# Performance work log

Measured on AMD Instinct MI355X. Metric: run time of the kernel, lower is better.

## Reference

```python
import jax, jax.numpy as jnp
import numpy as np

TOP_K = 2
EPS = 1e-10


def setup_inputs() -> dict:
    key = jax.random.key(0)
    k1, k2, k3, k4 = jax.random.split(key, 4)
    B, S, H, E = 4, 2048, 1024, 8
    tokens = jax.random.normal(k1, (B, S, H), dtype=jnp.float32)
    router_w = jax.random.normal(k2, (E, H), dtype=jnp.float32) * (1.0 / np.sqrt(H))
    router_b = jax.random.normal(k3, (E,), dtype=jnp.float32) * 0.01
    expert_weights = jax.random.normal(k4, (E, H, H), dtype=jnp.float32) * (1.0 / np.sqrt(H))
    return {"tokens": tokens, "router_w": router_w, "router_b": router_b,
            "expert_weights": expert_weights}


def reference(tokens, router_w, router_b, expert_weights):
    B, S, H = tokens.shape
    E = expert_weights.shape[0]
    # Router (torch Linear: x @ W^T + b)
    logits = jnp.einsum('bsh,eh->bse', tokens, router_w) + router_b  # [B,S,E]
    probs = jax.nn.softmax(logits, axis=-1)
    top_p, top_i = jax.lax.top_k(probs, TOP_K)            # [B,S,K]
    w = top_p / (jnp.sum(top_p, axis=-1, keepdims=True) + EPS)  # normalized weights

    x = tokens.reshape(-1, H)                              # [N,H]
    idx = top_i.reshape(-1, TOP_K)                         # [N,K]
    wf = w.reshape(-1, TOP_K)                              # [N,K]

    # Expert GEMM: compute all experts then gather selected (dense, vectorized
    # equivalent of the sort/pad/grouped-GEMM dispatch; padded rows with
    # original_indices==-1 never contribute to the output).
    y_all = jnp.einsum('nh,ehd->ned', x, expert_weights)   # [N,E,H]
    y_k = jnp.take_along_axis(y_all, idx[:, :, None], axis=1)  # [N,K,H]

    out = jnp.einsum('nk,nkh->nh', wf, y_k)                # weighted combine
    acc = jnp.clip(jnp.sum(wf, axis=-1), EPS, None)        # weight accumulator
    out = (out / acc[:, None]).reshape(B, S, H)

    # epsilon scale tying output to normalized router probs (gradient path)
    scale = 1.0 + jnp.sum(w, axis=-1, keepdims=True) * EPS  # [B,S,1]
    return out * scale
```

## Files before the change

kernel.cpp:

```cpp
#include <hip/hip_runtime.h>
#include <stdint.h>

#define N_TOK 8192
#define H_DIM 1024
#define N_EXP 8
#define MAX_TILES 136

typedef __bf16 bf16x8 __attribute__((ext_vector_type(8)));
typedef float floatx4 __attribute__((ext_vector_type(4)));

typedef __attribute__((address_space(1))) void GV;
typedef __attribute__((address_space(3))) void LV;

static __device__ __forceinline__ unsigned short f2b(float f) {
    union { float f; unsigned int i; } v; v.f = f;
    unsigned int u = v.i;
    return (unsigned short)((u + 0x7FFFu + ((u >> 16) & 1u)) >> 16);
}
static __device__ __forceinline__ float b2f(unsigned short u) {
    union { unsigned int i; float f; } v; v.i = ((unsigned int)u) << 16; return v.f;
}

__global__ __launch_bounds__(256) void k_front(
    const float* __restrict__ tokens,
    const float* __restrict__ router_w,
    const float* __restrict__ router_b,
    const float* __restrict__ W,
    int* __restrict__ sel, float* __restrict__ w_arr,
    unsigned short* __restrict__ tokb,
    unsigned short* __restrict__ Bp)
{
    const int t = threadIdx.x;

    if (blockIdx.x >= 2048) {
        const int idx = blockIdx.x - 2048;
        const int kg = idx & 127;
        const int e  = idx >> 7;
        const int d  = t * 4;
        const float* src = W + ((size_t)e * H_DIM + kg * 8) * H_DIM + d;
        float col[8][4];
#pragma unroll
        for (int j = 0; j < 8; ++j) {
            float4 v = *(const float4*)(src + (size_t)j * H_DIM);
            col[j][0] = v.x; col[j][1] = v.y; col[j][2] = v.z; col[j][3] = v.w;
        }
        unsigned short* dst = Bp + ((size_t)(e * 128 + kg) * H_DIM + d) * 8;
#pragma unroll
        for (int k = 0; k < 4; ++k) {
            unsigned short v[8];
#pragma unroll
            for (int j = 0; j < 8; ++j) v[j] = f2b(col[j][k]);
            *(uint4*)(dst + (size_t)k * 8) = *(uint4*)v;
        }
        return;
    }

    const int wave = t >> 6;
    const int lane = t & 63;
    const int n = blockIdx.x * 4 + wave;

    const float* xp = tokens + (size_t)n * H_DIM + lane * 16;
    float x[16];
#pragma unroll
    for (int i = 0; i < 4; ++i) {
        float4 v = *(const float4*)(xp + i * 4);
        x[i * 4 + 0] = v.x; x[i * 4 + 1] = v.y; x[i * 4 + 2] = v.z; x[i * 4 + 3] = v.w;
    }

    {
        unsigned short xb[16];
#pragma unroll
        for (int j = 0; j < 16; ++j) xb[j] = f2b(x[j]);
        unsigned short* dp = tokb + (size_t)n * H_DIM + lane * 16;
        *(uint4*)(dp)     = *(uint4*)(xb);
        *(uint4*)(dp + 8) = *(uint4*)(xb + 8);
    }

    float acc[N_EXP];
#pragma unroll
    for (int e = 0; e < N_EXP; ++e) {
        const float* wp = router_w + e * H_DIM + lane * 16;
        float s = 0.f;
#pragma unroll
        for (int i = 0; i < 4; ++i) {
            float4 v = *(const float4*)(wp + i * 4);
            s += x[i * 4 + 0] * v.x + x[i * 4 + 1] * v.y
               + x[i * 4 + 2] * v.z + x[i * 4 + 3] * v.w;
        }
        acc[e] = s;
    }

#pragma unroll
    for (int e = 0; e < N_EXP; ++e) {
        float a = acc[e];
#pragma unroll
        for (int off = 32; off > 0; off >>= 1) a += __shfl_xor(a, off);
        acc[e] = a;
    }

    if (lane == 0) {
        float lg[N_EXP];
#pragma unroll
        for (int e = 0; e < N_EXP; ++e) lg[e] = acc[e] + router_b[e];
        int e0 = 0;
#pragma unroll
        for (int e = 1; e < N_EXP; ++e) if (lg[e] > lg[e0]) e0 = e;
        int e1 = -1;
#pragma unroll
        for (int e = 0; e < N_EXP; ++e) {
            if (e == e0) continue;
            if (e1 < 0 || lg[e] > lg[e1]) e1 = e;
        }
        float w0 = 1.f / (1.f + __expf(lg[e1] - lg[e0]));
        float w1 = 1.f - w0;
        sel[n] = e0 | (e1 << 4);
        w_arr[n * 2] = w0;
        w_arr[n * 2 + 1] = w1;
    }
}

__global__ __launch_bounds__(256) void k_scan(
    const int* __restrict__ sel, int* __restrict__ cnt, int* __restrict__ bucket)
{
    __shared__ int ssel[N_TOK + N_TOK / 32];
    __shared__ int sc[256];
    const int e = blockIdx.x;
    const int t = threadIdx.x;
#pragma unroll
    for (int i = 0; i < 32; ++i) {
        int n = i * 256 + t;
        ssel[n + (n >> 5)] = sel[n];
    }
    __syncthreads();
    const int base = t * 32;
    int c = 0;
#pragma unroll
    for (int i = 0; i < 32; ++i) {
        int n = base + i;
        int s = ssel[n + (n >> 5)];
        c += ((s & 15) == e) + (((s >> 4) & 15) == e);
    }
    sc[t] = c;
    __syncthreads();
    for (int off = 1; off < 256; off <<= 1) {
        int v = (t >= off) ? sc[t - off] : 0;
        __syncthreads();
        sc[t] += v;
        __syncthreads();
    }
    int pos = sc[t] - c;
    if (t == 255) cnt[e] = sc[255];
#pragma unroll
    for (int i = 0; i < 32; ++i) {
        int n = base + i;
        int s = ssel[n + (n >> 5)];
        if ((s & 15) == e)        bucket[e * N_TOK + pos++] = 2 * n;
        if (((s >> 4) & 15) == e) bucket[e * N_TOK + pos++] = 2 * n + 1;
    }
}

__global__ __launch_bounds__(256, 2) void k_gemm(
    const unsigned short* __restrict__ tokb,
    const unsigned short* __restrict__ Bp,
    const int* __restrict__ cnt, const int* __restrict__ bucket,
    unsigned short* __restrict__ Y)
{
    const int nt = blockIdx.x & 7;
    const int tile = blockIdx.x >> 3;
    int base = 0, e = 0, mt = -1;
#pragma unroll
    for (int ee = 0; ee < 8; ++ee) {
        int te = (cnt[ee] + 127) >> 7;
        if (tile >= base && tile < base + te) { e = ee; mt = tile - base; }
        base += te;
    }
    if (mt < 0) return;
    const int cnt_local = cnt[e] - mt * 128;

    __shared__ __align__(16) unsigned short Asm[2][128 * 64];
    __shared__ __align__(16) unsigned short Bsm[2][8 * 128 * 8];
    __shared__ int rows[128];

    const int t = threadIdx.x;
    if (t < 128)
        rows[t] = (t < cnt_local) ? bucket[e * N_TOK + mt * 128 + t] : -1;
    __syncthreads();

    const int wv = t >> 6, lane = t & 63;
    const int d0 = nt * 128;

    const int p_sw = (lane & 7) ^ ((lane >> 3) & 7);
    const unsigned short* aptr[4];
#pragma unroll
    for (int i = 0; i < 4; ++i) {
        int r = i * 32 + wv * 8 + (lane >> 3);
        int rid = rows[r];
        int tok = (rid >= 0) ? (rid >> 1) : 0;
        aptr[i] = tokb + (size_t)tok * H_DIM + p_sw * 8;
    }
    const unsigned short* bbase = Bp
        + ((size_t)(e * 128 + (t >> 7)) * H_DIM + d0 + (t & 127)) * 8;

    const int w_row = wv >> 1, w_col = wv & 1;
    const int m_lane = lane & 15, quad = lane >> 4;
    const int r7 = m_lane & 7;

    floatx4 acc[4][4];
#pragma unroll
    for (int i = 0; i < 4; ++i)
#pragma unroll
        for (int j = 0; j < 4; ++j) acc[i][j] = (floatx4){0.f, 0.f, 0.f, 0.f};

#pragma unroll
    for (int i = 0; i < 4; ++i) {
        __builtin_amdgcn_global_load_lds(
            (GV*)(aptr[i]), (LV*)(&Asm[0][i * 2048 + wv * 512]), 16, 0, 0);
        __builtin_amdgcn_global_load_lds(
            (GV*)(bbase + (size_t)i * 16384), (LV*)(&Bsm[0][i * 2048 + wv * 512]), 16, 0, 0);
    }
    asm volatile("s_waitcnt vmcnt(0)" ::: "memory");
    __builtin_amdgcn_s_barrier();
    asm volatile("" ::: "memory");

    for (int kt = 0; kt < H_DIM / 64; ++kt) {
        const int cb = kt & 1;
        if (kt < H_DIM / 64 - 1) {
#pragma unroll
            for (int i = 0; i < 4; ++i) {
                __builtin_amdgcn_global_load_lds(
                    (GV*)(aptr[i] + (kt + 1) * 64),
                    (LV*)(&Asm[cb ^ 1][i * 2048 + wv * 512]), 16, 0, 0);
                __builtin_amdgcn_global_load_lds(
                    (GV*)(bbase + (size_t)i * 16384 + (size_t)(kt + 1) * 65536),
                    (LV*)(&Bsm[cb ^ 1][i * 2048 + wv * 512]), 16, 0, 0);
            }
        }

#pragma unroll
        for (int s = 0; s < 2; ++s) {
            bf16x8 a[4], b[4];
#pragma unroll
            for (int i = 0; i < 4; ++i) {
                int row = w_row * 64 + i * 16 + m_lane;
                a[i] = *(const bf16x8*)&Asm[cb][row * 64 + ((s * 4 + quad) ^ r7) * 8];
            }
#pragma unroll
            for (int j = 0; j < 4; ++j)
                b[j] = *(const bf16x8*)&Bsm[cb][((s * 4 + quad) * 128 + w_col * 64 + j * 16 + m_lane) * 8];
#pragma unroll
            for (int i = 0; i < 4; ++i)
#pragma unroll
                for (int j = 0; j < 4; ++j)
                    acc[i][j] = __builtin_amdgcn_mfma_f32_16x16x32_bf16(a[i], b[j], acc[i][j], 0, 0, 0);
        }

        asm volatile("s_waitcnt vmcnt(0)" ::: "memory");
        __builtin_amdgcn_s_barrier();
        asm volatile("" ::: "memory");
    }

#pragma unroll
    for (int i = 0; i < 4; ++i) {
        const int lr_base = w_row * 64 + i * 16 + quad * 4;
#pragma unroll
        for (int reg = 0; reg < 4; ++reg) {
            const int lr = lr_base + reg;
            const int rid = rows[lr];
            if (rid >= 0) {
                unsigned short v[4];
#pragma unroll
                for (int j = 0; j < 4; ++j) v[j] = f2b(acc[i][j][reg]);
                *(uint2*)(Y + (size_t)rid * H_DIM + d0 + w_col * 64 + m_lane * 4) = *(uint2*)v;
            }
        }
    }
}

__global__ __launch_bounds__(256) void k_combine(
    const unsigned short* __restrict__ Y, const float* __restrict__ w_arr,
    float* __restrict__ out)
{
    __shared__ __align__(16) unsigned short Ys[4 * H_DIM];
    const int t = threadIdx.x;
    const int b = blockIdx.x;
    const int wv = t >> 6, lane = t & 63;
    const unsigned short* src = Y + (size_t)b * 4 * H_DIM;
#pragma unroll
    for (int r = 0; r < 2; ++r) {
        __builtin_amdgcn_global_load_lds(
            (GV*)(src + (size_t)r * 2048 + wv * 512 + lane * 8),
            (LV*)(&Ys[r * 2048 + wv * 512]), 16, 0, 0);
    }
    __syncthreads();

    const int tok = t >> 7;
    const int n = 2 * b + tok;
    const int d0 = (t & 127) * 8;
    const int seg = d0 >> 7;
    const int dseg = d0 & 127;
    const int wc = dseg >> 6;
    const int j  = (dseg >> 4) & 3;
    const int m0 = dseg & 15;
    const int sbase = tok * 2 * H_DIM + seg * 128 + wc * 64 + j;
    const float w0 = w_arr[2 * n], w1 = w_arr[2 * n + 1];

    float o[8];
#pragma unroll
    for (int k = 0; k < 8; ++k) {
        int s = sbase + (m0 + k) * 4;
        o[k] = w0 * b2f(Ys[s]) + w1 * b2f(Ys[s + H_DIM]);
    }
    float4* op = (float4*)(out + (size_t)n * H_DIM + d0);
    op[0] = make_float4(o[0], o[1], o[2], o[3]);
    op[1] = make_float4(o[4], o[5], o[6], o[7]);
}

extern "C" void kernel_launch(void* const* d_in, const int* in_sizes, int n_in,
                              void* d_out, int out_size, void* d_ws, size_t ws_size,
                              hipStream_t stream)
{
    const float* tokens   = (const float*)d_in[0];
    const float* router_w = (const float*)d_in[1];
    const float* router_b = (const float*)d_in[2];
    const float* W        = (const float*)d_in[3];
    float* out = (float*)d_out;

    char* ws = (char*)d_ws;
    int*   cnt    = (int*)(ws);
    int*   sel    = (int*)(ws + 1024);
    float* w_arr  = (float*)(ws + 34816);
    int*   bucket = (int*)(ws + 100352);
    unsigned short* tokb = (unsigned short*)(ws + 362496);
    unsigned short* Bp   = (unsigned short*)(ws + 17139712);
    unsigned short* Y    = (unsigned short*)(ws + 33916928);

    k_front  <<<2048 + 1024, 256, 0, stream>>>(tokens, router_w, router_b, W,
                                               sel, w_arr, tokb, Bp);
    k_scan   <<<N_EXP, 256, 0, stream>>>(sel, cnt, bucket);
    k_gemm   <<<MAX_TILES * 8, 256, 0, stream>>>(tokb, Bp, cnt, bucket, Y);
    k_combine<<<N_TOK * (H_DIM / 8) / 256, 256, 0, stream>>>(Y, w_arr, out);
}
```

Baseline: 218.1 us.

## Shrink grouped GEMM tiles to 64x128 with persistent grid-stride scheduling

The expert GEMM moves from 128x128 tiles with 256 threads to 64x128 tiles with 128 threads, launched on a fixed persistent grid of 1056 blocks that loop over work items. The smaller M tile is meant to cut padding waste in each expert's last tile and to allow three blocks per CU. In exchange it drops LDS double buffering, so each k-step loads and then computes behind two barriers. It also halves A-tile reuse per B load and reads bucket indices straight from global memory instead of shared memory.

```diff
diff --git a/kernel.cpp b/kernel.cpp
--- a/kernel.cpp
+++ b/kernel.cpp
@@ -4,7 +4,7 @@
 #define N_TOK 8192
 #define H_DIM 1024
 #define N_EXP 8
-#define MAX_TILES 136
+#define GEMM_GRID 1056
 
 typedef __bf16 bf16x8 __attribute__((ext_vector_type(8)));
 typedef float floatx4 __attribute__((ext_vector_type(4)));
@@ -159,118 +159,105 @@
     }
 }
 
-__global__ __launch_bounds__(256, 2) void k_gemm(
+__global__ __launch_bounds__(128, 3) void k_gemm(
     const unsigned short* __restrict__ tokb,
     const unsigned short* __restrict__ Bp,
     const int* __restrict__ cnt, const int* __restrict__ bucket,
     unsigned short* __restrict__ Y)
 {
-    const int nt = blockIdx.x & 7;
-    const int tile = blockIdx.x >> 3;
-    int base = 0, e = 0, mt = -1;
-#pragma unroll
-    for (int ee = 0; ee < 8; ++ee) {
-        int te = (cnt[ee] + 127) >> 7;
-        if (tile >= base && tile < base + te) { e = ee; mt = tile - base; }
-        base += te;
-    }
-    if (mt < 0) return;
-    const int cnt_local = cnt[e] - mt * 128;
-
-    __shared__ __align__(16) unsigned short Asm[2][128 * 64];
-    __shared__ __align__(16) unsigned short Bsm[2][8 * 128 * 8];
-    __shared__ int rows[128];
+    __shared__ __align__(16) unsigned short Asm[64 * 64];
+    __shared__ __align__(16) unsigned short Bsm[8 * 128 * 8];
 
     const int t = threadIdx.x;
-    if (t < 128)
-        rows[t] = (t < cnt_local) ? bucket[e * N_TOK + mt * 128 + t] : -1;
-    __syncthreads();
-
     const int wv = t >> 6, lane = t & 63;
-    const int d0 = nt * 128;
-
+    const int m_lane = lane & 15, quad = lane >> 4;
     const int p_sw = (lane & 7) ^ ((lane >> 3) & 7);
-    const unsigned short* aptr[4];
-#pragma unroll
-    for (int i = 0; i < 4; ++i) {
-        int r = i * 32 + wv * 8 + (lane >> 3);
-        int rid = rows[r];
-        int tok = (rid >= 0) ? (rid >> 1) : 0;
-        aptr[i] = tokb + (size_t)tok * H_DIM + p_sw * 8;
-    }
-    const unsigned short* bbase = Bp
-        + ((size_t)(e * 128 + (t >> 7)) * H_DIM + d0 + (t & 127)) * 8;
-
-    const int w_row = wv >> 1, w_col = wv & 1;
-    const int m_lane = lane & 15, quad = lane >> 4;
-    const int r7 = m_lane & 7;
-
-    floatx4 acc[4][4];
-#pragma unroll
-    for (int i = 0; i < 4; ++i)
-#pragma unroll
-        for (int j = 0; j < 4; ++j) acc[i][j] = (floatx4){0.f, 0.f, 0.f, 0.f};
-
-#pragma unroll
-    for (int i = 0; i < 4; ++i) {
-        __builtin_amdgcn_global_load_lds(
-            (GV*)(aptr[i]), (LV*)(&Asm[0][i * 2048 + wv * 512]), 16, 0, 0);
-        __builtin_amdgcn_global_load_lds(
-            (GV*)(bbase + (size_t)i * 16384), (LV*)(&Bsm[0][i * 2048 + wv * 512]), 16, 0, 0);
-    }
-    asm volatile("s_waitcnt vmcnt(0)" ::: "memory");
-    __builtin_amdgcn_s_barrier();
-    asm volatile("" ::: "memory");
-
-    for (int kt = 0; kt < H_DIM / 64; ++kt) {
-        const int cb = kt & 1;
-        if (kt < H_DIM / 64 - 1) {
-#pragma unroll
-            for (int i = 0; i < 4; ++i) {
+
+    int cs[N_EXP];
+#pragma unroll
+    for (int ee = 0; ee < N_EXP; ++ee) cs[ee] = cnt[ee];
+    int n_t64 = 0;
+#pragma unroll
+    for (int ee = 0; ee < N_EXP; ++ee) n_t64 += (cs[ee] + 63) >> 6;
+    const int n_it = n_t64 * 8;
+
+    for (int item = blockIdx.x; item < n_it; item += GEMM_GRID) {
+        const int t64 = item >> 3;
+        const int nt  = item & 7;
+        int base = 0, e = 0, mt = 0;
+#pragma unroll
+        for (int ee = 0; ee < N_EXP; ++ee) {
+            int te = (cs[ee] + 63) >> 6;
+            if (t64 >= base && t64 < base + te) { e = ee; mt = t64 - base; }
+            base += te;
+        }
+        const int cnt_local = cs[e] - mt * 64;
+        const int d0 = nt * 128;
+        const int* bk = bucket + e * N_TOK + mt * 64;
+
+        const unsigned short* aptr[4];
+#pragma unroll
+        for (int i = 0; i < 4; ++i) {
+            int r = i * 16 + wv * 8 + (lane >> 3);
+            int rid = (r < cnt_local) ? bk[r] : -1;
+            int tok = (rid >= 0) ? (rid >> 1) : 0;
+            aptr[i] = tokb + (size_t)tok * H_DIM + p_sw * 8;
+        }
+        const unsigned short* bbase = Bp
+            + ((size_t)(e * 128) * H_DIM + d0 + wv * 64 + lane) * 8;
+
+        floatx4 acc[4][4];
+#pragma unroll
+        for (int i = 0; i < 4; ++i)
+#pragma unroll
+            for (int j = 0; j < 4; ++j) acc[i][j] = (floatx4){0.f, 0.f, 0.f, 0.f};
+
+        for (int kt = 0; kt < H_DIM / 64; ++kt) {
+#pragma unroll
+            for (int i = 0; i < 4; ++i)
                 __builtin_amdgcn_global_load_lds(
-                    (GV*)(aptr[i] + (kt + 1) * 64),
-                    (LV*)(&Asm[cb ^ 1][i * 2048 + wv * 512]), 16, 0, 0);
+                    (GV*)(aptr[i] + kt * 64),
+                    (LV*)(&Asm[i * 1024 + wv * 512]), 16, 0, 0);
+#pragma unroll
+            for (int i = 0; i < 8; ++i)
                 __builtin_amdgcn_global_load_lds(
-                    (GV*)(bbase + (size_t)i * 16384 + (size_t)(kt + 1) * 65536),
-                    (LV*)(&Bsm[cb ^ 1][i * 2048 + wv * 512]), 16, 0, 0);
+                    (GV*)(bbase + (size_t)(kt * 8 + i) * (H_DIM * 8)),
+                    (LV*)(&Bsm[i * 1024 + wv * 512]), 16, 0, 0);
+            __syncthreads();
+
+#pragma unroll
+            for (int s = 0; s < 2; ++s) {
+                bf16x8 a[4], b[4];
+#pragma unroll
+                for (int i = 0; i < 4; ++i) {
+                    int row = i * 16 + m_lane;
+                    a[i] = *(const bf16x8*)&Asm[row * 64 + ((s * 4 + quad) ^ (m_lane & 7)) * 8];
+                }
+#pragma unroll
+                for (int j = 0; j < 4; ++j)
+                    b[j] = *(const bf16x8*)&Bsm[((s * 4 + quad) * 128 + wv * 64 + j * 16 + m_lane) * 8];
+#pragma unroll
+                for (int i = 0; i < 4; ++i)
+#pragma unroll
+                    for (int j = 0; j < 4; ++j)
+                        acc[i][j] = __builtin_amdgcn_mfma_f32_16x16x32_bf16(a[i], b[j], acc[i][j], 0, 0, 0);
             }
-        }
-
-#pragma unroll
-        for (int s = 0; s < 2; ++s) {
-            bf16x8 a[4], b[4];
-#pragma unroll
-            for (int i = 0; i < 4; ++i) {
-                int row = w_row * 64 + i * 16 + m_lane;
-                a[i] = *(const bf16x8*)&Asm[cb][row * 64 + ((s * 4 + quad) ^ r7) * 8];
-            }
-#pragma unroll
-            for (int j = 0; j < 4; ++j)
-                b[j] = *(const bf16x8*)&Bsm[cb][((s * 4 + quad) * 128 + w_col * 64 + j * 16 + m_lane) * 8];
-#pragma unroll
-            for (int i = 0; i < 4; ++i)
-#pragma unroll
-                for (int j = 0; j < 4; ++j)
-                    acc[i][j] = __builtin_amdgcn_mfma_f32_16x16x32_bf16(a[i], b[j], acc[i][j], 0, 0, 0);
-        }
-
-        asm volatile("s_waitcnt vmcnt(0)" ::: "memory");
-        __builtin_amdgcn_s_barrier();
-        asm volatile("" ::: "memory");
-    }
-
-#pragma unroll
-    for (int i = 0; i < 4; ++i) {
-        const int lr_base = w_row * 64 + i * 16 + quad * 4;
-#pragma unroll
-        for (int reg = 0; reg < 4; ++reg) {
-            const int lr = lr_base + reg;
-            const int rid = rows[lr];
-            if (rid >= 0) {
-                unsigned short v[4];
-#pragma unroll
-                for (int j = 0; j < 4; ++j) v[j] = f2b(acc[i][j][reg]);
-                *(uint2*)(Y + (size_t)rid * H_DIM + d0 + w_col * 64 + m_lane * 4) = *(uint2*)v;
+            __syncthreads();
+        }
+
+#pragma unroll
+        for (int i = 0; i < 4; ++i) {
+            const int lr_base = i * 16 + quad * 4;
+#pragma unroll
+            for (int reg = 0; reg < 4; ++reg) {
+                const int lr = lr_base + reg;
+                const int rid = (lr < cnt_local) ? bk[lr] : -1;
+                if (rid >= 0) {
+                    unsigned short v[4];
+#pragma unroll
+                    for (int j = 0; j < 4; ++j) v[j] = f2b(acc[i][j][reg]);
+                    *(uint2*)(Y + (size_t)rid * H_DIM + d0 + wv * 64 + m_lane * 4) = *(uint2*)v;
+                }
             }
         }
     }
@@ -337,6 +324,6 @@
     k_front  <<<2048 + 1024, 256, 0, stream>>>(tokens, router_w, router_b, W,
                                                sel, w_arr, tokb, Bp);
     k_scan   <<<N_EXP, 256, 0, stream>>>(sel, cnt, bucket);
-    k_gemm   <<<MAX_TILES * 8, 256, 0, stream>>>(tokb, Bp, cnt, bucket, Y);
+    k_gemm   <<<GEMM_GRID, 128, 0, stream>>>(tokb, Bp, cnt, bucket, Y);
     k_combine<<<N_TOK * (H_DIM / 8) / 256, 256, 0, stream>>>(Y, w_arr, out);
 }
```

New measurement: 202.4 us. 1.08x faster.
